# Optimization experiments

Hardware: AMD Instinct MI355X
Metric: run time of the kernel (lower is better)

Reference implementation:

```python
import jax, jax.numpy as jnp
import numpy as np
from jax import lax

B, T, D, NH = 8, 2048, 128, 4
HD = D // NH
EPS = 1e-5


def _ln(x, g, b):
    m = x.mean(-1, keepdims=True)
    v = ((x - m) ** 2).mean(-1, keepdims=True)
    return (x - m) / jnp.sqrt(v + EPS) * g + b


def _gelu(x):  # exact (erf) GELU, matching torch nn.GELU default
    return jax.nn.gelu(x, approximate=False)


def _forward(lob_feat, trade_feat, has_trade,
             ei_w, ei_b, ei_g, ei_beta, decay,
             in_proj_w, in_proj_b, out_proj_w, out_proj_b,
             cn_g, cn_b,
             lob_w, lob_b, lob_g, lob_beta,
             tr_w, tr_b, tr_g, tr_beta,
             of_w, of_b, of_g, of_beta):
    # event impact: Linear -> LayerNorm -> Tanh, gated by has_trade
    impact = jnp.tanh(_ln(trade_feat @ ei_w.T + ei_b, ei_g, ei_beta))
    impact = impact * has_trade[..., None]              # [B,T,D]

    # diagonal linear recurrence: state_t = sigmoid(decay) * state_{t-1} + impact_t
    d = jax.nn.sigmoid(decay)                           # [D]

    def step(s, x):
        s = d * s + x
        return s, s

    _, states = lax.scan(step, jnp.zeros_like(impact[:, 0]),
                         jnp.swapaxes(impact, 0, 1))    # [T,B,D]
    state_seq = jnp.swapaxes(states, 0, 1)              # [B,T,D]

    # fusion MLPs (dropout is identity in eval)
    lob_enh = _gelu(_ln(jnp.concatenate([lob_feat, state_seq], -1) @ lob_w.T + lob_b,
                        lob_g, lob_beta))
    trade_enh = _gelu(_ln(jnp.concatenate([trade_feat, state_seq], -1) @ tr_w.T + tr_b,
                          tr_g, tr_beta))

    # torch nn.MultiheadAttention (batch_first): q=lob_enh, k=v=trade_enh
    wq, wk, wv = in_proj_w[:D], in_proj_w[D:2 * D], in_proj_w[2 * D:]
    bq, bk, bv = in_proj_b[:D], in_proj_b[D:2 * D], in_proj_b[2 * D:]
    q = (lob_enh @ wq.T + bq).reshape(B, T, NH, HD)
    k = (trade_enh @ wk.T + bk).reshape(B, T, NH, HD)
    v = (trade_enh @ wv.T + bv).reshape(B, T, NH, HD)
    scores = jnp.einsum('bqhd,bkhd->bhqk', q, k) / jnp.sqrt(jnp.float32(HD))
    attn = jax.nn.softmax(scores, axis=-1)
    ctx = jnp.einsum('bhqk,bkhd->bqhd', attn, v).reshape(B, T, D)
    fused_attn = ctx @ out_proj_w.T + out_proj_b

    fused = _ln(lob_enh + fused_attn, cn_g, cn_b)
    output = _gelu(_ln(jnp.concatenate([fused, trade_enh], -1) @ of_w.T + of_b,
                       of_g, of_beta))
    return output


def setup_inputs() -> dict:
    key = jax.random.key(0)
    ks = jax.random.split(key, 20)
    s1 = 1.0 / np.sqrt(D)
    s2 = 1.0 / np.sqrt(2 * D)
    return {
        'lob_feat': jax.random.normal(ks[0], (B, T, D), jnp.float32),
        'trade_feat': jax.random.normal(ks[1], (B, T, D), jnp.float32),
        'has_trade': (jax.random.uniform(ks[2], (B, T)) < 0.5).astype(jnp.float32),
        'ei_w': jax.random.normal(ks[3], (D, D), jnp.float32) * s1,
        'ei_b': jnp.zeros((D,), jnp.float32),
        'ei_g': jnp.ones((D,), jnp.float32),
        'ei_beta': jnp.zeros((D,), jnp.float32),
        'decay': jnp.ones((D,), jnp.float32) * 0.9,
        'in_proj_w': jax.random.normal(ks[4], (3 * D, D), jnp.float32) * s1,
        'in_proj_b': jnp.zeros((3 * D,), jnp.float32),
        'out_proj_w': jax.random.normal(ks[5], (D, D), jnp.float32) * s1,
        'out_proj_b': jnp.zeros((D,), jnp.float32),
        'cn_g': jnp.ones((D,), jnp.float32),
        'cn_b': jnp.zeros((D,), jnp.float32),
        'lob_w': jax.random.normal(ks[6], (D, 2 * D), jnp.float32) * s2,
        'lob_b': jnp.zeros((D,), jnp.float32),
        'lob_g': jnp.ones((D,), jnp.float32),
        'lob_beta': jnp.zeros((D,), jnp.float32),
        'tr_w': jax.random.normal(ks[7], (D, 2 * D), jnp.float32) * s2,
        'tr_b': jnp.zeros((D,), jnp.float32),
        'tr_g': jnp.ones((D,), jnp.float32),
        'tr_beta': jnp.zeros((D,), jnp.float32),
        'of_w': jax.random.normal(ks[8], (D, 2 * D), jnp.float32) * s2,
        'of_b': jnp.zeros((D,), jnp.float32),
        'of_g': jnp.ones((D,), jnp.float32),
        'of_beta': jnp.zeros((D,), jnp.float32),
    }


def reference(lob_feat, trade_feat, has_trade,
              ei_w, ei_b, ei_g, ei_beta, decay,
              in_proj_w, in_proj_b, out_proj_w, out_proj_b,
              cn_g, cn_b,
              lob_w, lob_b, lob_g, lob_beta,
              tr_w, tr_b, tr_g, tr_beta,
              of_w, of_b, of_g, of_beta):
    return _forward(lob_feat, trade_feat, has_trade,
                    ei_w, ei_b, ei_g, ei_beta, decay,
                    in_proj_w, in_proj_b, out_proj_w, out_proj_b,
                    cn_g, cn_b,
                    lob_w, lob_b, lob_g, lob_beta,
                    tr_w, tr_b, tr_g, tr_beta,
                    of_w, of_b, of_g, of_beta)
```

## Files before the change

kernel.cpp:

```cpp
#include <hip/hip_runtime.h>
#include <math.h>


#define T_  2048

typedef short bf16x8 __attribute__((ext_vector_type(8)));
typedef float f32x4  __attribute__((ext_vector_type(4)));
typedef unsigned short ushort_t;

__device__ __forceinline__ float sigm(float x) { return 1.0f / (1.0f + __expf(-x)); }

__device__ __forceinline__ unsigned short f2bf(float x) {
    union { float f; unsigned u; } v; v.f = x;
    unsigned r = v.u + 0x7FFFu + ((v.u >> 16) & 1u);
    return (unsigned short)(r >> 16);
}
__device__ __forceinline__ float bf2f(ushort_t u) {
    union { unsigned u; float f; } v; v.u = ((unsigned)u) << 16; return v.f;
}

__device__ __forceinline__ float gelu_f(float x) {
    const float e = exp2f(fmaf(0.044715f * x, x * x, x) * -2.3022083f);
    return x * __builtin_amdgcn_rcpf(1.0f + e);
}
__device__ __forceinline__ float tanh_f(float y) {
    const float e = exp2f(y * 2.8853900818f);
    return 1.0f - 2.0f * __builtin_amdgcn_rcpf(e + 1.0f);
}
#define MX3(a, b, c) fmaxf(fmaxf((a), (b)), (c))

__global__ __launch_bounds__(256) void prep_kernel(
    const float* __restrict__ lob, const float* __restrict__ trade,
    const float* __restrict__ eiw, const float* __restrict__ ipw,
    const float* __restrict__ opw, const float* __restrict__ lobw,
    const float* __restrict__ trw, const float* __restrict__ ofw,
    ushort_t* __restrict__ pool)
{
    const size_t i8 = ((size_t)blockIdx.x * 256 + threadIdx.x) * 8;
    const float* src; size_t off;
    if      (i8 < 2097152) { src = lob;   off = 0; }
    else if (i8 < 4194304) { src = trade; off = 2097152; }
    else if (i8 < 4210688) { src = eiw;   off = 4194304; }
    else if (i8 < 4259840) { src = ipw;   off = 4210688; }
    else if (i8 < 4276224) { src = opw;   off = 4259840; }
    else if (i8 < 4308992) { src = lobw;  off = 4276224; }
    else if (i8 < 4341760) { src = trw;   off = 4308992; }
    else                   { src = ofw;   off = 4341760; }
    const float4 a = *(const float4*)(src + (i8 - off));
    const float4 b = *(const float4*)(src + (i8 - off) + 4);
    bf16x8 o;
    o[0] = (short)f2bf(a.x); o[1] = (short)f2bf(a.y);
    o[2] = (short)f2bf(a.z); o[3] = (short)f2bf(a.w);
    o[4] = (short)f2bf(b.x); o[5] = (short)f2bf(b.y);
    o[6] = (short)f2bf(b.z); o[7] = (short)f2bf(b.w);
    *(bf16x8*)(pool + i8) = o;
}

__global__ __launch_bounds__(256) void gemm_ei(
    const ushort_t* __restrict__ Xb0, const ushort_t* __restrict__ Wb,
    const float* __restrict__ bias, const float* __restrict__ gamma,
    const float* __restrict__ beta, const float* __restrict__ extra,
    ushort_t* __restrict__ outb)
{
    __shared__ float red[32][2][2];
    const int tid = threadIdx.x, wid = tid >> 6, lane = tid & 63;
    const int c2 = lane & 15, g = lane >> 4;
    const int rowblk = wid >> 1, chf = wid & 1, cb0 = chf * 4;
    const int R0 = blockIdx.x * 32 + rowblk * 16;

    f32x4 acc[4] = {};
#pragma unroll
    for (int ch = 0; ch < 4; ch++) {
        const bf16x8 a = *(const bf16x8*)(Xb0 + (size_t)(R0 + c2) * 128 + ch * 32 + g * 8);
#pragma unroll
        for (int j = 0; j < 4; j++) {
            const bf16x8 b = *(const bf16x8*)(Wb + (size_t)((cb0 + j) * 16 + c2) * 128 + ch * 32 + g * 8);
            acc[j] = __builtin_amdgcn_mfma_f32_16x16x32_bf16(a, b, acc[j], 0, 0, 0);
        }
    }
    float gm[4], bt[4];
#pragma unroll
    for (int j = 0; j < 4; j++) {
        const int col = (cb0 + j) * 16 + c2;
        const float bb = bias[col];
        gm[j] = gamma[col]; bt[j] = beta[col];
#pragma unroll
        for (int r = 0; r < 4; r++) acc[j][r] += bb;
    }
#pragma unroll
    for (int r = 0; r < 4; r++) {
        float s = 0.f, ss = 0.f;
#pragma unroll
        for (int j = 0; j < 4; j++) { const float v = acc[j][r]; s += v; ss = fmaf(v, v, ss); }
#pragma unroll
        for (int o = 8; o; o >>= 1) { s += __shfl_xor(s, o); ss += __shfl_xor(ss, o); }
        if (c2 == 0) {
            red[rowblk * 16 + 4 * g + r][chf][0] = s;
            red[rowblk * 16 + 4 * g + r][chf][1] = ss;
        }
    }
    __syncthreads();
#pragma unroll
    for (int r = 0; r < 4; r++) {
        const int lr = rowblk * 16 + 4 * g + r;
        const float S  = red[lr][0][0] + red[lr][1][0];
        const float SS = red[lr][0][1] + red[lr][1][1];
        const float mean = S * (1.0f / 128.0f);
        float var = SS * (1.0f / 128.0f) - mean * mean;
        var = fmaxf(var, 0.0f);
        const float rstd = rsqrtf(var + 1e-5f);
        const int R = blockIdx.x * 32 + lr;
        const float ext = extra[R];
#pragma unroll
        for (int j = 0; j < 4; j++) {
            const float y = (acc[j][r] - mean) * rstd * gm[j] + bt[j];
            outb[(size_t)R * 128 + (cb0 + j) * 16 + c2] = f2bf(tanh_f(y) * ext);
        }
    }
}

__global__ __launch_bounds__(256) void enh_qkv(
    const ushort_t* __restrict__ lobb, const ushort_t* __restrict__ trab,
    const ushort_t* __restrict__ stab,
    const ushort_t* __restrict__ lobw, const ushort_t* __restrict__ trw,
    const ushort_t* __restrict__ ipw, const float* __restrict__ ipb,
    const float* __restrict__ lob_b, const float* __restrict__ lob_g,
    const float* __restrict__ lob_beta,
    const float* __restrict__ tr_b, const float* __restrict__ tr_g,
    const float* __restrict__ tr_beta,
    ushort_t* __restrict__ lobe_b, ushort_t* __restrict__ tre_bf,
    ushort_t* __restrict__ qo, ushort_t* __restrict__ ko, ushort_t* __restrict__ vo)
{
    __shared__ ushort_t lob_t[32][136];
    __shared__ ushort_t tre_t[32][136];
    __shared__ ushort_t vls[128][36];
    __shared__ float red[32][2][4];
    const int tid = threadIdx.x, wid = tid >> 6, lane = tid & 63;
    const int c2 = lane & 15, g = lane >> 4;
    const int rowblk = wid >> 1, chf = wid & 1, cb0 = chf * 4;
    const int RB = blockIdx.x * 32;
    const int R0 = RB + rowblk * 16;

    f32x4 aL[4] = {}, aT[4] = {};
#pragma unroll
    for (int ch = 0; ch < 8; ch++) {
        const int kk = (ch & 3) * 32;
        bf16x8 xl, xt;
        if (ch < 4) {
            xl = *(const bf16x8*)(lobb + (size_t)(R0 + c2) * 128 + kk + g * 8);
            xt = *(const bf16x8*)(trab + (size_t)(R0 + c2) * 128 + kk + g * 8);
        } else {
            xl = *(const bf16x8*)(stab + (size_t)(R0 + c2) * 128 + kk + g * 8);
            xt = xl;
        }
#pragma unroll
        for (int j = 0; j < 4; j++) {
            const size_t wo = (size_t)((cb0 + j) * 16 + c2) * 256 + ch * 32 + g * 8;
            aL[j] = __builtin_amdgcn_mfma_f32_16x16x32_bf16(xl, *(const bf16x8*)(lobw + wo), aL[j], 0, 0, 0);
            aT[j] = __builtin_amdgcn_mfma_f32_16x16x32_bf16(xt, *(const bf16x8*)(trw + wo), aT[j], 0, 0, 0);
        }
    }
#pragma unroll
    for (int j = 0; j < 4; j++) {
        const int col = (cb0 + j) * 16 + c2;
        const float bL = lob_b[col], bT = tr_b[col];
#pragma unroll
        for (int r = 0; r < 4; r++) { aL[j][r] += bL; aT[j][r] += bT; }
    }
#pragma unroll
    for (int r = 0; r < 4; r++) {
        float sL = 0.f, ssL = 0.f, sT = 0.f, ssT = 0.f;
#pragma unroll
        for (int j = 0; j < 4; j++) {
            const float vL = aL[j][r], vT = aT[j][r];
            sL += vL; ssL = fmaf(vL, vL, ssL);
            sT += vT; ssT = fmaf(vT, vT, ssT);
        }
#pragma unroll
        for (int o = 8; o; o >>= 1) {
            sL += __shfl_xor(sL, o); ssL += __shfl_xor(ssL, o);
            sT += __shfl_xor(sT, o); ssT += __shfl_xor(ssT, o);
        }
        if (c2 == 0) {
            float* rd = red[rowblk * 16 + 4 * g + r][chf];
            rd[0] = sL; rd[1] = ssL; rd[2] = sT; rd[3] = ssT;
        }
    }
    __syncthreads();
#pragma unroll
    for (int r = 0; r < 4; r++) {
        const int lr = rowblk * 16 + 4 * g + r;
        const int R = RB + lr;
        const float SL  = red[lr][0][0] + red[lr][1][0];
        const float SSL = red[lr][0][1] + red[lr][1][1];
        const float ST  = red[lr][0][2] + red[lr][1][2];
        const float SST = red[lr][0][3] + red[lr][1][3];
        const float mL = SL * (1.0f / 128.0f), mT = ST * (1.0f / 128.0f);
        const float rL = rsqrtf(fmaxf(SSL * (1.0f / 128.0f) - mL * mL, 0.0f) + 1e-5f);
        const float rT = rsqrtf(fmaxf(SST * (1.0f / 128.0f) - mT * mT, 0.0f) + 1e-5f);
#pragma unroll
        for (int j = 0; j < 4; j++) {
            const int col = (cb0 + j) * 16 + c2;
            const float yL = gelu_f((aL[j][r] - mL) * rL * lob_g[col] + lob_beta[col]);
            const float yT = gelu_f((aT[j][r] - mT) * rT * tr_g[col] + tr_beta[col]);
            const ushort_t lb = f2bf(yL);
            lobe_b[(size_t)R * 128 + col] = lb;
            lob_t[lr][col] = lb;
            const ushort_t tb = f2bf(yT);
            tre_bf[(size_t)R * 128 + col] = tb;
            tre_t[lr][col] = tb;
        }
    }
    __syncthreads();

    const float qscale = 0.17677669529663687f * 1.4426950408889634f;
#pragma unroll
    for (int which = 0; which < 3; which++) {
        const ushort_t (*src)[136] = (which == 0) ? lob_t : tre_t;
        const ushort_t* Wp = ipw + (size_t)which * 16384;
        f32x4 pa[4] = {};
#pragma unroll
        for (int ch = 0; ch < 4; ch++) {
            const bf16x8 a = *(const bf16x8*)&src[rowblk * 16 + c2][ch * 32 + g * 8];
#pragma unroll
            for (int j = 0; j < 4; j++) {
                const bf16x8 b = *(const bf16x8*)(Wp + (size_t)((cb0 + j) * 16 + c2) * 128 + ch * 32 + g * 8);
                pa[j] = __builtin_amdgcn_mfma_f32_16x16x32_bf16(a, b, pa[j], 0, 0, 0);
            }
        }
        if (which < 2) {
            ushort_t* dst = (which == 0) ? qo : ko;
            const float sc = (which == 0) ? qscale : 1.0f;
#pragma unroll
            for (int j = 0; j < 4; j++) {
                const int col = (cb0 + j) * 16 + c2;
                const float bb = ipb[which * 128 + col];
                const int h = col >> 5, hd = col & 31;
#pragma unroll
                for (int r = 0; r < 4; r++) {
                    const int R = R0 + 4 * g + r;
                    const int b = R >> 11, t = R & 2047;
                    dst[(((size_t)b * 4 + h) * 2048 + t) * 32 + hd] = f2bf((pa[j][r] + bb) * sc);
                }
            }
        } else {
#pragma unroll
            for (int j = 0; j < 4; j++) {
                const int col = (cb0 + j) * 16 + c2;
                const float bb = ipb[256 + col];
#pragma unroll
                for (int r = 0; r < 4; r++)
                    vls[col][rowblk * 16 + 4 * g + r] = f2bf(pa[j][r] + bb);
            }
        }
    }
    __syncthreads();
    {
        const int col = tid >> 1, hf = tid & 1;
        const int h = col >> 5, hd = col & 31;
        const int b = RB >> 11;
        unsigned w[8];
#pragma unroll
        for (int e = 0; e < 8; e++) {
            const int p0 = hf * 16 + 2 * e;
            const int g2 = p0 >> 3, j2 = p0 & 7;
            const int lk = 4 * g2 + j2 + (j2 >= 4 ? 12 : 0);
            w[e] = (unsigned)vls[col][lk] | ((unsigned)vls[col][lk + 1] << 16);
        }
        ushort_t* dst = vo + (((size_t)b * 4 + h) * 32 + hd) * 2048 + (RB & 2047) + hf * 16;
        *(uint4*)dst       = *(const uint4*)&w[0];
        *(uint4*)(dst + 8) = *(const uint4*)&w[4];
    }
}

__global__ __launch_bounds__(256) void attn_kernel(
    const ushort_t* __restrict__ q, const ushort_t* __restrict__ k,
    const ushort_t* __restrict__ vtg,
    ushort_t* __restrict__ part, float* __restrict__ rs_part,
    float* __restrict__ m_part)
{
    __shared__ ushort_t ks[2][64][40];
    __shared__ ushort_t vt[2][32][72];
    const int tid = threadIdx.x, wid = tid >> 6, lane = tid & 63;
    const int c = lane & 15, g = lane >> 4;
    const int half = blockIdx.x & 1, qt = blockIdx.x >> 1;
    const int bh = blockIdx.y, b = bh >> 2, h = bh & 3;
    const ushort_t* kb_ = k   + (size_t)bh * 65536 + (size_t)half * 1024 * 32;
    const ushort_t* vb_ = vtg + (size_t)bh * 65536 + (size_t)half * 1024;
    const int q0 = qt * 128 + wid * 32;

    const ushort_t* qbase = q + ((size_t)bh * 2048 + q0) * 32;
    const bf16x8 qf0 = *(const bf16x8*)(qbase + (size_t)c * 32 + g * 8);
    const bf16x8 qf1 = *(const bf16x8*)(qbase + (size_t)(16 + c) * 32 + g * 8);

    bf16x8 ones;
#pragma unroll
    for (int i = 0; i < 8; i++) ones[i] = (short)0x3F80;

    float m0 = 0.0f, m1 = 0.0f;
    f32x4 acc[2][2] = {};
    f32x4 racc[2] = {};

    const int srow = tid >> 2, ssg = tid & 3;
    const int vd = tid >> 3, vkg = tid & 7;

    {
        const bf16x8 kk8 = *(const bf16x8*)(kb_ + (size_t)srow * 32 + ssg * 8);
        const bf16x8 vv8 = *(const bf16x8*)(vb_ + (size_t)vd * 2048 + vkg * 8);
        *(bf16x8*)&ks[0][srow][ssg * 8] = kk8;
        *(bf16x8*)&vt[0][vd][vkg * 8] = vv8;
    }
    __syncthreads();

    for (int kt = 0; kt < 16; kt++) {
        const int cur = kt & 1;
        bf16x8 kk8, vv8;
        if (kt + 1 < 16) {
            kk8 = *(const bf16x8*)(kb_ + ((size_t)(kt + 1) * 64 + srow) * 32 + ssg * 8);
            vv8 = *(const bf16x8*)(vb_ + (size_t)vd * 2048 + (kt + 1) * 64 + vkg * 8);
        }

        f32x4 s0[4], s1[4];
        __builtin_amdgcn_s_setprio(1);
#pragma unroll
        for (int kb2 = 0; kb2 < 4; kb2++) {
            const bf16x8 kf = *(const bf16x8*)&ks[cur][kb2 * 16 + c][g * 8];
            f32x4 z = {};
            s0[kb2] = __builtin_amdgcn_mfma_f32_16x16x32_bf16(kf, qf0, z, 0, 0, 0);
            s1[kb2] = __builtin_amdgcn_mfma_f32_16x16x32_bf16(kf, qf1, z, 0, 0, 0);
        }
        __builtin_amdgcn_s_setprio(0);

        float lm = MX3(s0[0][0], s0[0][1], s0[0][2]);
        lm = MX3(lm, s0[0][3], s0[1][0]);
        lm = MX3(lm, s0[1][1], s0[1][2]);
        lm = MX3(lm, s0[1][3], s0[2][0]);
        lm = MX3(lm, s0[2][1], s0[2][2]);
        lm = MX3(lm, s0[2][3], s0[3][0]);
        lm = MX3(lm, s0[3][1], s0[3][2]);
        lm = MX3(lm, s0[3][3], s1[0][0]);
        lm = MX3(lm, s1[0][1], s1[0][2]);
        lm = MX3(lm, s1[0][3], s1[1][0]);
        lm = MX3(lm, s1[1][1], s1[1][2]);
        lm = MX3(lm, s1[1][3], s1[2][0]);
        lm = MX3(lm, s1[2][1], s1[2][2]);
        lm = MX3(lm, s1[2][3], s1[3][0]);
        lm = MX3(lm, s1[3][1], s1[3][2]);
        lm = fmaxf(lm, s1[3][3]);
        if (__any(lm > 80.0f || m0 != 0.0f || m1 != 0.0f)) {
            float l0 = -1e30f, l1 = -1e30f;
#pragma unroll
            for (int kb2 = 0; kb2 < 4; kb2++) {
#pragma unroll
                for (int r = 0; r < 4; r++) { l0 = fmaxf(l0, s0[kb2][r]); l1 = fmaxf(l1, s1[kb2][r]); }
            }
            l0 = fmaxf(l0, __shfl_xor(l0, 16)); l0 = fmaxf(l0, __shfl_xor(l0, 32));
            l1 = fmaxf(l1, __shfl_xor(l1, 16)); l1 = fmaxf(l1, __shfl_xor(l1, 32));
            const float n0 = fmaxf(m0, l0), n1 = fmaxf(m1, l1);
            const float a0 = exp2f(m0 - n0), a1 = exp2f(m1 - n1);
#pragma unroll
            for (int nb = 0; nb < 2; nb++)
#pragma unroll
                for (int r = 0; r < 4; r++) { acc[0][nb][r] *= a0; acc[1][nb][r] *= a1; }
#pragma unroll
            for (int r = 0; r < 4; r++) { racc[0][r] *= a0; racc[1][r] *= a1; }
            m0 = n0; m1 = n1;
#pragma unroll
            for (int kb2 = 0; kb2 < 4; kb2++)
#pragma unroll
                for (int r = 0; r < 4; r++) {
                    s0[kb2][r] = exp2f(s0[kb2][r] - m0);
                    s1[kb2][r] = exp2f(s1[kb2][r] - m1);
                }
        } else {
#pragma unroll
            for (int kb2 = 0; kb2 < 4; kb2++)
#pragma unroll
                for (int r = 0; r < 4; r++) {
                    s0[kb2][r] = exp2f(s0[kb2][r]);
                    s1[kb2][r] = exp2f(s1[kb2][r]);
                }
        }

        union { unsigned u[4]; bf16x8 v; } p0a, p0b, p1a, p1b;
        asm("v_cvt_pk_bf16_f32 %0, %1, %2" : "=v"(p0a.u[0]) : "v"(s0[0][0]), "v"(s0[0][1]));
        asm("v_cvt_pk_bf16_f32 %0, %1, %2" : "=v"(p0a.u[1]) : "v"(s0[0][2]), "v"(s0[0][3]));
        asm("v_cvt_pk_bf16_f32 %0, %1, %2" : "=v"(p0a.u[2]) : "v"(s0[1][0]), "v"(s0[1][1]));
        asm("v_cvt_pk_bf16_f32 %0, %1, %2" : "=v"(p0a.u[3]) : "v"(s0[1][2]), "v"(s0[1][3]));
        asm("v_cvt_pk_bf16_f32 %0, %1, %2" : "=v"(p0b.u[0]) : "v"(s0[2][0]), "v"(s0[2][1]));
        asm("v_cvt_pk_bf16_f32 %0, %1, %2" : "=v"(p0b.u[1]) : "v"(s0[2][2]), "v"(s0[2][3]));
        asm("v_cvt_pk_bf16_f32 %0, %1, %2" : "=v"(p0b.u[2]) : "v"(s0[3][0]), "v"(s0[3][1]));
        asm("v_cvt_pk_bf16_f32 %0, %1, %2" : "=v"(p0b.u[3]) : "v"(s0[3][2]), "v"(s0[3][3]));
        asm("v_cvt_pk_bf16_f32 %0, %1, %2" : "=v"(p1a.u[0]) : "v"(s1[0][0]), "v"(s1[0][1]));
        asm("v_cvt_pk_bf16_f32 %0, %1, %2" : "=v"(p1a.u[1]) : "v"(s1[0][2]), "v"(s1[0][3]));
        asm("v_cvt_pk_bf16_f32 %0, %1, %2" : "=v"(p1a.u[2]) : "v"(s1[1][0]), "v"(s1[1][1]));
        asm("v_cvt_pk_bf16_f32 %0, %1, %2" : "=v"(p1a.u[3]) : "v"(s1[1][2]), "v"(s1[1][3]));
        asm("v_cvt_pk_bf16_f32 %0, %1, %2" : "=v"(p1b.u[0]) : "v"(s1[2][0]), "v"(s1[2][1]));
        asm("v_cvt_pk_bf16_f32 %0, %1, %2" : "=v"(p1b.u[1]) : "v"(s1[2][2]), "v"(s1[2][3]));
        asm("v_cvt_pk_bf16_f32 %0, %1, %2" : "=v"(p1b.u[2]) : "v"(s1[3][0]), "v"(s1[3][1]));
        asm("v_cvt_pk_bf16_f32 %0, %1, %2" : "=v"(p1b.u[3]) : "v"(s1[3][2]), "v"(s1[3][3]));

        __builtin_amdgcn_s_setprio(1);
#pragma unroll
        for (int nb = 0; nb < 2; nb++) {
            const bf16x8 v0 = *(const bf16x8*)&vt[cur][nb * 16 + c][g * 8];
            const bf16x8 v1 = *(const bf16x8*)&vt[cur][nb * 16 + c][32 + g * 8];
            acc[0][nb] = __builtin_amdgcn_mfma_f32_16x16x32_bf16(v0, p0a.v, acc[0][nb], 0, 0, 0);
            acc[0][nb] = __builtin_amdgcn_mfma_f32_16x16x32_bf16(v1, p0b.v, acc[0][nb], 0, 0, 0);
            acc[1][nb] = __builtin_amdgcn_mfma_f32_16x16x32_bf16(v0, p1a.v, acc[1][nb], 0, 0, 0);
            acc[1][nb] = __builtin_amdgcn_mfma_f32_16x16x32_bf16(v1, p1b.v, acc[1][nb], 0, 0, 0);
        }
        racc[0] = __builtin_amdgcn_mfma_f32_16x16x32_bf16(ones, p0a.v, racc[0], 0, 0, 0);
        racc[0] = __builtin_amdgcn_mfma_f32_16x16x32_bf16(ones, p0b.v, racc[0], 0, 0, 0);
        racc[1] = __builtin_amdgcn_mfma_f32_16x16x32_bf16(ones, p1a.v, racc[1], 0, 0, 0);
        racc[1] = __builtin_amdgcn_mfma_f32_16x16x32_bf16(ones, p1b.v, racc[1], 0, 0, 0);
        __builtin_amdgcn_s_setprio(0);

        if (kt + 1 < 16) {
            *(bf16x8*)&ks[cur ^ 1][srow][ssg * 8] = kk8;
            *(bf16x8*)&vt[cur ^ 1][vd][vkg * 8] = vv8;
        }
        __syncthreads();
    }

    ushort_t* pb = part + (size_t)half * 2097152;
#pragma unroll
    for (int qf = 0; qf < 2; qf++) {
        const int qrow = q0 + qf * 16 + c;
        ushort_t* dst = pb + ((size_t)(b * 2048 + qrow)) * 128 + h * 32;
#pragma unroll
        for (int nb = 0; nb < 2; nb++) {
            unsigned w0, w1;
            asm("v_cvt_pk_bf16_f32 %0, %1, %2" : "=v"(w0) : "v"(acc[qf][nb][0]), "v"(acc[qf][nb][1]));
            asm("v_cvt_pk_bf16_f32 %0, %1, %2" : "=v"(w1) : "v"(acc[qf][nb][2]), "v"(acc[qf][nb][3]));
            uint2 wv; wv.x = w0; wv.y = w1;
            *(uint2*)(dst + nb * 16 + 4 * g) = wv;
        }
    }
    if (g == 0) {
        float* rsp = rs_part + (size_t)(half * 32 + bh) * 2048;
        float* mp  = m_part  + (size_t)(half * 32 + bh) * 2048;
        rsp[q0 + c]      = racc[0][0];
        rsp[q0 + 16 + c] = racc[1][0];
        mp[q0 + c]       = m0;
        mp[q0 + 16 + c]  = m1;
    }
}

__global__ __launch_bounds__(256) void out_fuse(
    const ushort_t* __restrict__ ctxA, const ushort_t* __restrict__ ctxB,
    const float* __restrict__ rs_part, const float* __restrict__ m_part,
    const ushort_t* __restrict__ treb,
    const ushort_t* __restrict__ opw, const float* __restrict__ opb,
    const float* __restrict__ cn_g, const float* __restrict__ cn_b,
    const ushort_t* __restrict__ ofw, const float* __restrict__ of_b,
    const float* __restrict__ of_g, const float* __restrict__ of_beta,
    const ushort_t* __restrict__ lobe_b, float* __restrict__ out)
{
    __shared__ ushort_t fus_t[32][136];
    __shared__ float red[32][2][2];
    const int tid = threadIdx.x, wid = tid >> 6, lane = tid & 63;
    const int c2 = lane & 15, g = lane >> 4;
    const int rowblk = wid >> 1, chf = wid & 1, cb0 = chf * 4;
    const int RB = blockIdx.x * 32;
    const int R0 = RB + rowblk * 16;

    const int rowA = R0 + c2;
    const int bb2 = rowA >> 11, tt = rowA & 2047;
    float fA[4], fB[4];
#pragma unroll
    for (int h = 0; h < 4; h++) {
        const int bh = bb2 * 4 + h;
        const float mA = m_part[(size_t)bh * 2048 + tt];
        const float mB = m_part[(size_t)(32 + bh) * 2048 + tt];
        const float rA = rs_part[(size_t)bh * 2048 + tt];
        const float rB = rs_part[(size_t)(32 + bh) * 2048 + tt];
        const float M = fmaxf(mA, mB);
        const float wA = exp2f(mA - M), wB = exp2f(mB - M);
        const float inv = __builtin_amdgcn_rcpf(fmaf(rA, wA, rB * wB));
        fA[h] = wA * inv; fB[h] = wB * inv;
    }

    f32x4 acc[4] = {};
#pragma unroll
    for (int ch = 0; ch < 4; ch++) {
        const bf16x8 aA = *(const bf16x8*)(ctxA + (size_t)rowA * 128 + ch * 32 + g * 8);
        const bf16x8 aB = *(const bf16x8*)(ctxB + (size_t)rowA * 128 + ch * 32 + g * 8);
        union { unsigned u[4]; bf16x8 v; } am;
#pragma unroll
        for (int i = 0; i < 4; i++) {
            const float e0 = bf2f((ushort_t)aA[2 * i]) * fA[ch] + bf2f((ushort_t)aB[2 * i]) * fB[ch];
            const float e1 = bf2f((ushort_t)aA[2 * i + 1]) * fA[ch] + bf2f((ushort_t)aB[2 * i + 1]) * fB[ch];
            asm("v_cvt_pk_bf16_f32 %0, %1, %2" : "=v"(am.u[i]) : "v"(e0), "v"(e1));
        }
#pragma unroll
        for (int j = 0; j < 4; j++) {
            const bf16x8 b = *(const bf16x8*)(opw + (size_t)((cb0 + j) * 16 + c2) * 128 + ch * 32 + g * 8);
            acc[j] = __builtin_amdgcn_mfma_f32_16x16x32_bf16(am.v, b, acc[j], 0, 0, 0);
        }
    }
#pragma unroll
    for (int j = 0; j < 4; j++) {
        const int col = (cb0 + j) * 16 + c2;
        const float bb = opb[col];
#pragma unroll
        for (int r = 0; r < 4; r++)
            acc[j][r] += bb + bf2f(lobe_b[(size_t)(R0 + 4 * g + r) * 128 + col]);
    }
#pragma unroll
    for (int r = 0; r < 4; r++) {
        float s = 0.f, ss = 0.f;
#pragma unroll
        for (int j = 0; j < 4; j++) { const float v = acc[j][r]; s += v; ss = fmaf(v, v, ss); }
#pragma unroll
        for (int o = 8; o; o >>= 1) { s += __shfl_xor(s, o); ss += __shfl_xor(ss, o); }
        if (c2 == 0) {
            red[rowblk * 16 + 4 * g + r][chf][0] = s;
            red[rowblk * 16 + 4 * g + r][chf][1] = ss;
        }
    }
    __syncthreads();
#pragma unroll
    for (int r = 0; r < 4; r++) {
        const int lr = rowblk * 16 + 4 * g + r;
        const float S  = red[lr][0][0] + red[lr][1][0];
        const float SS = red[lr][0][1] + red[lr][1][1];
        const float mean = S * (1.0f / 128.0f);
        const float rstd = rsqrtf(fmaxf(SS * (1.0f / 128.0f) - mean * mean, 0.0f) + 1e-5f);
#pragma unroll
        for (int j = 0; j < 4; j++) {
            const int col = (cb0 + j) * 16 + c2;
            fus_t[lr][col] = f2bf((acc[j][r] - mean) * rstd * cn_g[col] + cn_b[col]);
        }
    }
    __syncthreads();

    f32x4 a2[4] = {};
#pragma unroll
    for (int ch = 0; ch < 8; ch++) {
        bf16x8 a;
        if (ch < 4) a = *(const bf16x8*)&fus_t[rowblk * 16 + c2][ch * 32 + g * 8];
        else        a = *(const bf16x8*)(treb + (size_t)(R0 + c2) * 128 + (ch - 4) * 32 + g * 8);
#pragma unroll
        for (int j = 0; j < 4; j++) {
            const bf16x8 b = *(const bf16x8*)(ofw + (size_t)((cb0 + j) * 16 + c2) * 256 + ch * 32 + g * 8);
            a2[j] = __builtin_amdgcn_mfma_f32_16x16x32_bf16(a, b, a2[j], 0, 0, 0);
        }
    }
#pragma unroll
    for (int j = 0; j < 4; j++) {
        const float bb = of_b[(cb0 + j) * 16 + c2];
#pragma unroll
        for (int r = 0; r < 4; r++) a2[j][r] += bb;
    }
#pragma unroll
    for (int r = 0; r < 4; r++) {
        float s = 0.f, ss = 0.f;
#pragma unroll
        for (int j = 0; j < 4; j++) { const float v = a2[j][r]; s += v; ss = fmaf(v, v, ss); }
#pragma unroll
        for (int o = 8; o; o >>= 1) { s += __shfl_xor(s, o); ss += __shfl_xor(ss, o); }
        if (c2 == 0) {
            red[rowblk * 16 + 4 * g + r][chf][0] = s;
            red[rowblk * 16 + 4 * g + r][chf][1] = ss;
        }
    }
    __syncthreads();
#pragma unroll
    for (int r = 0; r < 4; r++) {
        const int lr = rowblk * 16 + 4 * g + r;
        const float S  = red[lr][0][0] + red[lr][1][0];
        const float SS = red[lr][0][1] + red[lr][1][1];
        const float mean = S * (1.0f / 128.0f);
        const float rstd = rsqrtf(fmaxf(SS * (1.0f / 128.0f) - mean * mean, 0.0f) + 1e-5f);
        const int R = RB + lr;
#pragma unroll
        for (int j = 0; j < 4; j++) {
            const int col = (cb0 + j) * 16 + c2;
            const float y = (a2[j][r] - mean) * rstd * of_g[col] + of_beta[col];
            out[(size_t)R * 128 + col] = gelu_f(y);
        }
    }
}

__global__ void scan_ends_kernel(const ushort_t* __restrict__ imp,
                                 const float* __restrict__ decay,
                                 float* __restrict__ ends)
{
    const int c = threadIdx.x;
    const int ch = blockIdx.x, b = blockIdx.y;
    const float d = sigm(decay[c]);
    const size_t base = ((size_t)b * T_ + ch * 64) * 128 + c;
    float s = 0.0f;
#pragma unroll 4
    for (int tl = 0; tl < 64; tl++)
        s = fmaf(d, s, bf2f(imp[base + (size_t)tl * 128]));
    ends[((size_t)b * 32 + ch) * 128 + c] = s;
}

__global__ void scan_carry_kernel(const float* __restrict__ ends,
                                  const float* __restrict__ decay,
                                  float* __restrict__ carry)
{
    const int c = threadIdx.x;
    const int b = blockIdx.x;
    const float d = sigm(decay[c]);
    float dl = d;
#pragma unroll
    for (int i = 0; i < 6; i++) dl *= dl;
    float e = 0.0f;
#pragma unroll
    for (int ch = 0; ch < 32; ch++) {
        carry[((size_t)b * 32 + ch) * 128 + c] = e;
        e = fmaf(dl, e, ends[((size_t)b * 32 + ch) * 128 + c]);
    }
}

__global__ void scan_fin_kernel(const ushort_t* __restrict__ imp,
                                const float* __restrict__ decay,
                                const float* __restrict__ carry,
                                ushort_t* __restrict__ stbf)
{
    const int c = threadIdx.x;
    const int ch = blockIdx.x, b = blockIdx.y;
    const float d = sigm(decay[c]);
    float s = carry[((size_t)b * 32 + ch) * 128 + c];
    const size_t base = ((size_t)b * T_ + ch * 64) * 128 + c;
#pragma unroll 4
    for (int tl = 0; tl < 64; tl++) {
        s = fmaf(d, s, bf2f(imp[base + (size_t)tl * 128]));
        stbf[base + (size_t)tl * 128] = f2bf(s);
    }
}

extern "C" void kernel_launch(void* const* d_in, const int* in_sizes, int n_in,
                              void* d_out, int out_size, void* d_ws, size_t ws_size,
                              hipStream_t stream)
{
    const float* lob_feat   = (const float*)d_in[0];
    const float* trade_feat = (const float*)d_in[1];
    const float* has_trade  = (const float*)d_in[2];
    const float* ei_w       = (const float*)d_in[3];
    const float* ei_b       = (const float*)d_in[4];
    const float* ei_g       = (const float*)d_in[5];
    const float* ei_beta    = (const float*)d_in[6];
    const float* decay      = (const float*)d_in[7];
    const float* in_proj_w  = (const float*)d_in[8];
    const float* in_proj_b  = (const float*)d_in[9];
    const float* out_proj_w = (const float*)d_in[10];
    const float* out_proj_b = (const float*)d_in[11];
    const float* cn_g       = (const float*)d_in[12];
    const float* cn_b       = (const float*)d_in[13];
    const float* lob_w      = (const float*)d_in[14];
    const float* lob_b      = (const float*)d_in[15];
    const float* lob_g      = (const float*)d_in[16];
    const float* lob_beta   = (const float*)d_in[17];
    const float* tr_w       = (const float*)d_in[18];
    const float* tr_b       = (const float*)d_in[19];
    const float* tr_g       = (const float*)d_in[20];
    const float* tr_beta    = (const float*)d_in[21];
    const float* of_w       = (const float*)d_in[22];
    const float* of_b       = (const float*)d_in[23];
    const float* of_g       = (const float*)d_in[24];
    const float* of_beta    = (const float*)d_in[25];

    char* W = (char*)d_ws;
    const size_t MB = 1u << 20;
    ushort_t* lobe_b   = (ushort_t*)W;
    float*    carry    = (float*)(W + 8 * MB);
    float*    ends     = (float*)(W + 8 * MB + 256 * 1024);
    ushort_t* pool     = (ushort_t*)(W + 9 * MB);
    ushort_t* imp_bf   = (ushort_t*)(W + 18 * MB);
    ushort_t* state_bf = (ushort_t*)(W + 22 * MB);
    ushort_t* tre_bf   = (ushort_t*)(W + 26 * MB);
    ushort_t* q_bf     = (ushort_t*)(W + 30 * MB);
    ushort_t* k_bf     = (ushort_t*)(W + 34 * MB);
    ushort_t* vt_g     = (ushort_t*)(W + 38 * MB);
    ushort_t* part     = (ushort_t*)(W + 42 * MB);
    float*    rs_part  = (float*)(W + 50 * MB);
    float*    m_part   = (float*)(W + 50 * MB + 512 * 1024);

    ushort_t* lob_bf   = pool;
    ushort_t* trade_bf = pool + 2097152;
    ushort_t* eiw_bf   = pool + 4194304;
    ushort_t* ipw_bf   = pool + 4210688;
    ushort_t* opw_bf   = pool + 4259840;
    ushort_t* lobw_bf  = pool + 4276224;
    ushort_t* trw_bf   = pool + 4308992;
    ushort_t* ofw_bf   = pool + 4341760;

    ushort_t* ctxA = part;
    ushort_t* ctxB = part + 2097152;

    const dim3 blk(256);

    prep_kernel<<<dim3(2136), blk, 0, stream>>>(lob_feat, trade_feat, ei_w, in_proj_w,
                                                out_proj_w, lob_w, tr_w, of_w, pool);
    gemm_ei<<<dim3(512), blk, 0, stream>>>(trade_bf, eiw_bf, ei_b, ei_g, ei_beta,
                                           has_trade, imp_bf);
    scan_ends_kernel<<<dim3(32, 8), dim3(128), 0, stream>>>(imp_bf, decay, ends);
    scan_carry_kernel<<<dim3(8), dim3(128), 0, stream>>>(ends, decay, carry);
    scan_fin_kernel<<<dim3(32, 8), dim3(128), 0, stream>>>(imp_bf, decay, carry, state_bf);
    enh_qkv<<<dim3(512), blk, 0, stream>>>(lob_bf, trade_bf, state_bf, lobw_bf, trw_bf,
                                           ipw_bf, in_proj_b, lob_b, lob_g, lob_beta,
                                           tr_b, tr_g, tr_beta, lobe_b, tre_bf,
                                           q_bf, k_bf, vt_g);
    attn_kernel<<<dim3(32, 32), blk, 0, stream>>>(q_bf, k_bf, vt_g, part, rs_part, m_part);
    out_fuse<<<dim3(512), blk, 0, stream>>>(ctxA, ctxB, rs_part, m_part, tre_bf,
                                            opw_bf, out_proj_b, cn_g, cn_b,
                                            ofw_bf, of_b, of_g, of_beta, lobe_b, (float*)d_out);
}
```

Before: 139.7 us.

## Split attention keys into four chunks and process query halves sequentially

The attention kernel now splits the key dimension four ways instead of two, doubling the grid to 2048 blocks, each handling 512 keys. out_fuse merges four partial contexts with a log-sum-exp style reweighting. The inner loop also processes the two 16-row query fragments one after another rather than interleaved, which lowers live register pressure. The goal is higher occupancy and more parallelism on the attention stage. The cost is more partial-result traffic and a heavier merge, and the workspace is relaid out with imp_bf aliased onto the part buffer.

```diff
diff --git a/kernel.cpp b/kernel.cpp
--- a/kernel.cpp
+++ b/kernel.cpp
@@ -283,10 +283,10 @@
     __shared__ ushort_t vt[2][32][72];
     const int tid = threadIdx.x, wid = tid >> 6, lane = tid & 63;
     const int c = lane & 15, g = lane >> 4;
-    const int half = blockIdx.x & 1, qt = blockIdx.x >> 1;
+    const int kq = blockIdx.x & 3, qt = blockIdx.x >> 2;
     const int bh = blockIdx.y, b = bh >> 2, h = bh & 3;
-    const ushort_t* kb_ = k   + (size_t)bh * 65536 + (size_t)half * 1024 * 32;
-    const ushort_t* vb_ = vtg + (size_t)bh * 65536 + (size_t)half * 1024;
+    const ushort_t* kb_ = k   + (size_t)bh * 65536 + (size_t)kq * 512 * 32;
+    const ushort_t* vb_ = vtg + (size_t)bh * 65536 + (size_t)kq * 512;
     const int q0 = qt * 128 + wid * 32;
 
     const ushort_t* qbase = q + ((size_t)bh * 2048 + q0) * 32;
@@ -312,118 +312,144 @@
     }
     __syncthreads();
 
-    for (int kt = 0; kt < 16; kt++) {
+    for (int kt = 0; kt < 8; kt++) {
         const int cur = kt & 1;
         bf16x8 kk8, vv8;
-        if (kt + 1 < 16) {
+        if (kt + 1 < 8) {
             kk8 = *(const bf16x8*)(kb_ + ((size_t)(kt + 1) * 64 + srow) * 32 + ssg * 8);
             vv8 = *(const bf16x8*)(vb_ + (size_t)vd * 2048 + (kt + 1) * 64 + vkg * 8);
         }
 
-        f32x4 s0[4], s1[4];
-        __builtin_amdgcn_s_setprio(1);
-#pragma unroll
-        for (int kb2 = 0; kb2 < 4; kb2++) {
-            const bf16x8 kf = *(const bf16x8*)&ks[cur][kb2 * 16 + c][g * 8];
-            f32x4 z = {};
-            s0[kb2] = __builtin_amdgcn_mfma_f32_16x16x32_bf16(kf, qf0, z, 0, 0, 0);
-            s1[kb2] = __builtin_amdgcn_mfma_f32_16x16x32_bf16(kf, qf1, z, 0, 0, 0);
-        }
-        __builtin_amdgcn_s_setprio(0);
-
-        float lm = MX3(s0[0][0], s0[0][1], s0[0][2]);
-        lm = MX3(lm, s0[0][3], s0[1][0]);
-        lm = MX3(lm, s0[1][1], s0[1][2]);
-        lm = MX3(lm, s0[1][3], s0[2][0]);
-        lm = MX3(lm, s0[2][1], s0[2][2]);
-        lm = MX3(lm, s0[2][3], s0[3][0]);
-        lm = MX3(lm, s0[3][1], s0[3][2]);
-        lm = MX3(lm, s0[3][3], s1[0][0]);
-        lm = MX3(lm, s1[0][1], s1[0][2]);
-        lm = MX3(lm, s1[0][3], s1[1][0]);
-        lm = MX3(lm, s1[1][1], s1[1][2]);
-        lm = MX3(lm, s1[1][3], s1[2][0]);
-        lm = MX3(lm, s1[2][1], s1[2][2]);
-        lm = MX3(lm, s1[2][3], s1[3][0]);
-        lm = MX3(lm, s1[3][1], s1[3][2]);
-        lm = fmaxf(lm, s1[3][3]);
-        if (__any(lm > 80.0f || m0 != 0.0f || m1 != 0.0f)) {
-            float l0 = -1e30f, l1 = -1e30f;
+        {
+            f32x4 s[4];
+            __builtin_amdgcn_s_setprio(1);
 #pragma unroll
             for (int kb2 = 0; kb2 < 4; kb2++) {
-#pragma unroll
-                for (int r = 0; r < 4; r++) { l0 = fmaxf(l0, s0[kb2][r]); l1 = fmaxf(l1, s1[kb2][r]); }
-            }
-            l0 = fmaxf(l0, __shfl_xor(l0, 16)); l0 = fmaxf(l0, __shfl_xor(l0, 32));
-            l1 = fmaxf(l1, __shfl_xor(l1, 16)); l1 = fmaxf(l1, __shfl_xor(l1, 32));
-            const float n0 = fmaxf(m0, l0), n1 = fmaxf(m1, l1);
-            const float a0 = exp2f(m0 - n0), a1 = exp2f(m1 - n1);
-#pragma unroll
-            for (int nb = 0; nb < 2; nb++)
-#pragma unroll
-                for (int r = 0; r < 4; r++) { acc[0][nb][r] *= a0; acc[1][nb][r] *= a1; }
-#pragma unroll
-            for (int r = 0; r < 4; r++) { racc[0][r] *= a0; racc[1][r] *= a1; }
-            m0 = n0; m1 = n1;
-#pragma unroll
-            for (int kb2 = 0; kb2 < 4; kb2++)
-#pragma unroll
-                for (int r = 0; r < 4; r++) {
-                    s0[kb2][r] = exp2f(s0[kb2][r] - m0);
-                    s1[kb2][r] = exp2f(s1[kb2][r] - m1);
-                }
-        } else {
-#pragma unroll
-            for (int kb2 = 0; kb2 < 4; kb2++)
-#pragma unroll
-                for (int r = 0; r < 4; r++) {
-                    s0[kb2][r] = exp2f(s0[kb2][r]);
-                    s1[kb2][r] = exp2f(s1[kb2][r]);
-                }
-        }
-
-        union { unsigned u[4]; bf16x8 v; } p0a, p0b, p1a, p1b;
-        asm("v_cvt_pk_bf16_f32 %0, %1, %2" : "=v"(p0a.u[0]) : "v"(s0[0][0]), "v"(s0[0][1]));
-        asm("v_cvt_pk_bf16_f32 %0, %1, %2" : "=v"(p0a.u[1]) : "v"(s0[0][2]), "v"(s0[0][3]));
-        asm("v_cvt_pk_bf16_f32 %0, %1, %2" : "=v"(p0a.u[2]) : "v"(s0[1][0]), "v"(s0[1][1]));
-        asm("v_cvt_pk_bf16_f32 %0, %1, %2" : "=v"(p0a.u[3]) : "v"(s0[1][2]), "v"(s0[1][3]));
-        asm("v_cvt_pk_bf16_f32 %0, %1, %2" : "=v"(p0b.u[0]) : "v"(s0[2][0]), "v"(s0[2][1]));
-        asm("v_cvt_pk_bf16_f32 %0, %1, %2" : "=v"(p0b.u[1]) : "v"(s0[2][2]), "v"(s0[2][3]));
-        asm("v_cvt_pk_bf16_f32 %0, %1, %2" : "=v"(p0b.u[2]) : "v"(s0[3][0]), "v"(s0[3][1]));
-        asm("v_cvt_pk_bf16_f32 %0, %1, %2" : "=v"(p0b.u[3]) : "v"(s0[3][2]), "v"(s0[3][3]));
-        asm("v_cvt_pk_bf16_f32 %0, %1, %2" : "=v"(p1a.u[0]) : "v"(s1[0][0]), "v"(s1[0][1]));
-        asm("v_cvt_pk_bf16_f32 %0, %1, %2" : "=v"(p1a.u[1]) : "v"(s1[0][2]), "v"(s1[0][3]));
-        asm("v_cvt_pk_bf16_f32 %0, %1, %2" : "=v"(p1a.u[2]) : "v"(s1[1][0]), "v"(s1[1][1]));
-        asm("v_cvt_pk_bf16_f32 %0, %1, %2" : "=v"(p1a.u[3]) : "v"(s1[1][2]), "v"(s1[1][3]));
-        asm("v_cvt_pk_bf16_f32 %0, %1, %2" : "=v"(p1b.u[0]) : "v"(s1[2][0]), "v"(s1[2][1]));
-        asm("v_cvt_pk_bf16_f32 %0, %1, %2" : "=v"(p1b.u[1]) : "v"(s1[2][2]), "v"(s1[2][3]));
-        asm("v_cvt_pk_bf16_f32 %0, %1, %2" : "=v"(p1b.u[2]) : "v"(s1[3][0]), "v"(s1[3][1]));
-        asm("v_cvt_pk_bf16_f32 %0, %1, %2" : "=v"(p1b.u[3]) : "v"(s1[3][2]), "v"(s1[3][3]));
-
-        __builtin_amdgcn_s_setprio(1);
-#pragma unroll
-        for (int nb = 0; nb < 2; nb++) {
-            const bf16x8 v0 = *(const bf16x8*)&vt[cur][nb * 16 + c][g * 8];
-            const bf16x8 v1 = *(const bf16x8*)&vt[cur][nb * 16 + c][32 + g * 8];
-            acc[0][nb] = __builtin_amdgcn_mfma_f32_16x16x32_bf16(v0, p0a.v, acc[0][nb], 0, 0, 0);
-            acc[0][nb] = __builtin_amdgcn_mfma_f32_16x16x32_bf16(v1, p0b.v, acc[0][nb], 0, 0, 0);
-            acc[1][nb] = __builtin_amdgcn_mfma_f32_16x16x32_bf16(v0, p1a.v, acc[1][nb], 0, 0, 0);
-            acc[1][nb] = __builtin_amdgcn_mfma_f32_16x16x32_bf16(v1, p1b.v, acc[1][nb], 0, 0, 0);
-        }
-        racc[0] = __builtin_amdgcn_mfma_f32_16x16x32_bf16(ones, p0a.v, racc[0], 0, 0, 0);
-        racc[0] = __builtin_amdgcn_mfma_f32_16x16x32_bf16(ones, p0b.v, racc[0], 0, 0, 0);
-        racc[1] = __builtin_amdgcn_mfma_f32_16x16x32_bf16(ones, p1a.v, racc[1], 0, 0, 0);
-        racc[1] = __builtin_amdgcn_mfma_f32_16x16x32_bf16(ones, p1b.v, racc[1], 0, 0, 0);
-        __builtin_amdgcn_s_setprio(0);
-
-        if (kt + 1 < 16) {
+                const bf16x8 kf = *(const bf16x8*)&ks[cur][kb2 * 16 + c][g * 8];
+                f32x4 z = {};
+                s[kb2] = __builtin_amdgcn_mfma_f32_16x16x32_bf16(kf, qf0, z, 0, 0, 0);
+            }
+            __builtin_amdgcn_s_setprio(0);
+            const float t0 = MX3(s[0][0], s[0][1], s[0][2]);
+            const float t1 = MX3(s[0][3], s[1][0], s[1][1]);
+            const float t2 = MX3(s[1][2], s[1][3], s[2][0]);
+            const float t3 = MX3(s[2][1], s[2][2], s[2][3]);
+            const float t4 = MX3(s[3][0], s[3][1], s[3][2]);
+            const float lm = fmaxf(MX3(t0, t1, t2), MX3(t3, t4, s[3][3]));
+            if (__any(lm > 80.0f || m0 != 0.0f)) {
+                float l = lm;
+                l = fmaxf(l, __shfl_xor(l, 16));
+                l = fmaxf(l, __shfl_xor(l, 32));
+                const float n = fmaxf(m0, l);
+                const float a = exp2f(m0 - n);
+#pragma unroll
+                for (int nb = 0; nb < 2; nb++)
+#pragma unroll
+                    for (int r = 0; r < 4; r++) acc[0][nb][r] *= a;
+#pragma unroll
+                for (int r = 0; r < 4; r++) racc[0][r] *= a;
+                m0 = n;
+#pragma unroll
+                for (int kb2 = 0; kb2 < 4; kb2++)
+#pragma unroll
+                    for (int r = 0; r < 4; r++) s[kb2][r] = exp2f(s[kb2][r] - m0);
+            } else {
+#pragma unroll
+                for (int kb2 = 0; kb2 < 4; kb2++)
+#pragma unroll
+                    for (int r = 0; r < 4; r++) s[kb2][r] = exp2f(s[kb2][r]);
+            }
+            union { unsigned u[4]; bf16x8 v; } pa, pb;
+            asm("v_cvt_pk_bf16_f32 %0, %1, %2" : "=v"(pa.u[0]) : "v"(s[0][0]), "v"(s[0][1]));
+            asm("v_cvt_pk_bf16_f32 %0, %1, %2" : "=v"(pa.u[1]) : "v"(s[0][2]), "v"(s[0][3]));
+            asm("v_cvt_pk_bf16_f32 %0, %1, %2" : "=v"(pa.u[2]) : "v"(s[1][0]), "v"(s[1][1]));
+            asm("v_cvt_pk_bf16_f32 %0, %1, %2" : "=v"(pa.u[3]) : "v"(s[1][2]), "v"(s[1][3]));
+            asm("v_cvt_pk_bf16_f32 %0, %1, %2" : "=v"(pb.u[0]) : "v"(s[2][0]), "v"(s[2][1]));
+            asm("v_cvt_pk_bf16_f32 %0, %1, %2" : "=v"(pb.u[1]) : "v"(s[2][2]), "v"(s[2][3]));
+            asm("v_cvt_pk_bf16_f32 %0, %1, %2" : "=v"(pb.u[2]) : "v"(s[3][0]), "v"(s[3][1]));
+            asm("v_cvt_pk_bf16_f32 %0, %1, %2" : "=v"(pb.u[3]) : "v"(s[3][2]), "v"(s[3][3]));
+            __builtin_amdgcn_s_setprio(1);
+#pragma unroll
+            for (int nb = 0; nb < 2; nb++) {
+                const bf16x8 v0 = *(const bf16x8*)&vt[cur][nb * 16 + c][g * 8];
+                const bf16x8 v1 = *(const bf16x8*)&vt[cur][nb * 16 + c][32 + g * 8];
+                acc[0][nb] = __builtin_amdgcn_mfma_f32_16x16x32_bf16(v0, pa.v, acc[0][nb], 0, 0, 0);
+                acc[0][nb] = __builtin_amdgcn_mfma_f32_16x16x32_bf16(v1, pb.v, acc[0][nb], 0, 0, 0);
+            }
+            racc[0] = __builtin_amdgcn_mfma_f32_16x16x32_bf16(ones, pa.v, racc[0], 0, 0, 0);
+            racc[0] = __builtin_amdgcn_mfma_f32_16x16x32_bf16(ones, pb.v, racc[0], 0, 0, 0);
+            __builtin_amdgcn_s_setprio(0);
+        }
+
+        {
+            f32x4 s[4];
+            __builtin_amdgcn_s_setprio(1);
+#pragma unroll
+            for (int kb2 = 0; kb2 < 4; kb2++) {
+                const bf16x8 kf = *(const bf16x8*)&ks[cur][kb2 * 16 + c][g * 8];
+                f32x4 z = {};
+                s[kb2] = __builtin_amdgcn_mfma_f32_16x16x32_bf16(kf, qf1, z, 0, 0, 0);
+            }
+            __builtin_amdgcn_s_setprio(0);
+            const float t0 = MX3(s[0][0], s[0][1], s[0][2]);
+            const float t1 = MX3(s[0][3], s[1][0], s[1][1]);
+            const float t2 = MX3(s[1][2], s[1][3], s[2][0]);
+            const float t3 = MX3(s[2][1], s[2][2], s[2][3]);
+            const float t4 = MX3(s[3][0], s[3][1], s[3][2]);
+            const float lm = fmaxf(MX3(t0, t1, t2), MX3(t3, t4, s[3][3]));
+            if (__any(lm > 80.0f || m1 != 0.0f)) {
+                float l = lm;
+                l = fmaxf(l, __shfl_xor(l, 16));
+                l = fmaxf(l, __shfl_xor(l, 32));
+                const float n = fmaxf(m1, l);
+                const float a = exp2f(m1 - n);
+#pragma unroll
+                for (int nb = 0; nb < 2; nb++)
+#pragma unroll
+                    for (int r = 0; r < 4; r++) acc[1][nb][r] *= a;
+#pragma unroll
+                for (int r = 0; r < 4; r++) racc[1][r] *= a;
+                m1 = n;
+#pragma unroll
+                for (int kb2 = 0; kb2 < 4; kb2++)
+#pragma unroll
+                    for (int r = 0; r < 4; r++) s[kb2][r] = exp2f(s[kb2][r] - m1);
+            } else {
+#pragma unroll
+                for (int kb2 = 0; kb2 < 4; kb2++)
+#pragma unroll
+                    for (int r = 0; r < 4; r++) s[kb2][r] = exp2f(s[kb2][r]);
+            }
+            union { unsigned u[4]; bf16x8 v; } pa, pb;
+            asm("v_cvt_pk_bf16_f32 %0, %1, %2" : "=v"(pa.u[0]) : "v"(s[0][0]), "v"(s[0][1]));
+            asm("v_cvt_pk_bf16_f32 %0, %1, %2" : "=v"(pa.u[1]) : "v"(s[0][2]), "v"(s[0][3]));
+            asm("v_cvt_pk_bf16_f32 %0, %1, %2" : "=v"(pa.u[2]) : "v"(s[1][0]), "v"(s[1][1]));
+            asm("v_cvt_pk_bf16_f32 %0, %1, %2" : "=v"(pa.u[3]) : "v"(s[1][2]), "v"(s[1][3]));
+            asm("v_cvt_pk_bf16_f32 %0, %1, %2" : "=v"(pb.u[0]) : "v"(s[2][0]), "v"(s[2][1]));
+            asm("v_cvt_pk_bf16_f32 %0, %1, %2" : "=v"(pb.u[1]) : "v"(s[2][2]), "v"(s[2][3]));
+            asm("v_cvt_pk_bf16_f32 %0, %1, %2" : "=v"(pb.u[2]) : "v"(s[3][0]), "v"(s[3][1]));
+            asm("v_cvt_pk_bf16_f32 %0, %1, %2" : "=v"(pb.u[3]) : "v"(s[3][2]), "v"(s[3][3]));
+            __builtin_amdgcn_s_setprio(1);
+#pragma unroll
+            for (int nb = 0; nb < 2; nb++) {
+                const bf16x8 v0 = *(const bf16x8*)&vt[cur][nb * 16 + c][g * 8];
+                const bf16x8 v1 = *(const bf16x8*)&vt[cur][nb * 16 + c][32 + g * 8];
+                acc[1][nb] = __builtin_amdgcn_mfma_f32_16x16x32_bf16(v0, pa.v, acc[1][nb], 0, 0, 0);
+                acc[1][nb] = __builtin_amdgcn_mfma_f32_16x16x32_bf16(v1, pb.v, acc[1][nb], 0, 0, 0);
+            }
+            racc[1] = __builtin_amdgcn_mfma_f32_16x16x32_bf16(ones, pa.v, racc[1], 0, 0, 0);
+            racc[1] = __builtin_amdgcn_mfma_f32_16x16x32_bf16(ones, pb.v, racc[1], 0, 0, 0);
+            __builtin_amdgcn_s_setprio(0);
+        }
+
+        if (kt + 1 < 8) {
             *(bf16x8*)&ks[cur ^ 1][srow][ssg * 8] = kk8;
             *(bf16x8*)&vt[cur ^ 1][vd][vkg * 8] = vv8;
         }
         __syncthreads();
     }
 
-    ushort_t* pb = part + (size_t)half * 2097152;
+    ushort_t* pb = part + (size_t)kq * 2097152;
 #pragma unroll
     for (int qf = 0; qf < 2; qf++) {
         const int qrow = q0 + qf * 16 + c;
@@ -438,8 +464,8 @@
         }
     }
     if (g == 0) {
-        float* rsp = rs_part + (size_t)(half * 32 + bh) * 2048;
-        float* mp  = m_part  + (size_t)(half * 32 + bh) * 2048;
+        float* rsp = rs_part + (size_t)(kq * 32 + bh) * 2048;
+        float* mp  = m_part  + (size_t)(kq * 32 + bh) * 2048;
         rsp[q0 + c]      = racc[0][0];
         rsp[q0 + 16 + c] = racc[1][0];
         mp[q0 + c]       = m0;
@@ -448,7 +474,7 @@
 }
 
 __global__ __launch_bounds__(256) void out_fuse(
-    const ushort_t* __restrict__ ctxA, const ushort_t* __restrict__ ctxB,
+    const ushort_t* __restrict__ part,
     const float* __restrict__ rs_part, const float* __restrict__ m_part,
     const ushort_t* __restrict__ treb,
     const ushort_t* __restrict__ opw, const float* __restrict__ opb,
@@ -467,30 +493,41 @@
 
     const int rowA = R0 + c2;
     const int bb2 = rowA >> 11, tt = rowA & 2047;
-    float fA[4], fB[4];
+    float f[4][4];
 #pragma unroll
     for (int h = 0; h < 4; h++) {
         const int bh = bb2 * 4 + h;
-        const float mA = m_part[(size_t)bh * 2048 + tt];
-        const float mB = m_part[(size_t)(32 + bh) * 2048 + tt];
-        const float rA = rs_part[(size_t)bh * 2048 + tt];
-        const float rB = rs_part[(size_t)(32 + bh) * 2048 + tt];
-        const float M = fmaxf(mA, mB);
-        const float wA = exp2f(mA - M), wB = exp2f(mB - M);
-        const float inv = __builtin_amdgcn_rcpf(fmaf(rA, wA, rB * wB));
-        fA[h] = wA * inv; fB[h] = wB * inv;
+        float m[4], r[4];
+#pragma unroll
+        for (int s = 0; s < 4; s++) {
+            m[s] = m_part[(size_t)(s * 32 + bh) * 2048 + tt];
+            r[s] = rs_part[(size_t)(s * 32 + bh) * 2048 + tt];
+        }
+        const float M = fmaxf(fmaxf(m[0], m[1]), fmaxf(m[2], m[3]));
+        float w[4], den = 0.f;
+#pragma unroll
+        for (int s = 0; s < 4; s++) { w[s] = exp2f(m[s] - M); den = fmaf(r[s], w[s], den); }
+        const float inv = __builtin_amdgcn_rcpf(den);
+#pragma unroll
+        for (int s = 0; s < 4; s++) f[s][h] = w[s] * inv;
     }
 
     f32x4 acc[4] = {};
 #pragma unroll
     for (int ch = 0; ch < 4; ch++) {
-        const bf16x8 aA = *(const bf16x8*)(ctxA + (size_t)rowA * 128 + ch * 32 + g * 8);
-        const bf16x8 aB = *(const bf16x8*)(ctxB + (size_t)rowA * 128 + ch * 32 + g * 8);
+        bf16x8 a[4];
+#pragma unroll
+        for (int s = 0; s < 4; s++)
+            a[s] = *(const bf16x8*)(part + (size_t)s * 2097152 + (size_t)rowA * 128 + ch * 32 + g * 8);
         union { unsigned u[4]; bf16x8 v; } am;
 #pragma unroll
         for (int i = 0; i < 4; i++) {
-            const float e0 = bf2f((ushort_t)aA[2 * i]) * fA[ch] + bf2f((ushort_t)aB[2 * i]) * fB[ch];
-            const float e1 = bf2f((ushort_t)aA[2 * i + 1]) * fA[ch] + bf2f((ushort_t)aB[2 * i + 1]) * fB[ch];
+            float e0 = 0.f, e1 = 0.f;
+#pragma unroll
+            for (int s = 0; s < 4; s++) {
+                e0 = fmaf(bf2f((ushort_t)a[s][2 * i]), f[s][ch], e0);
+                e1 = fmaf(bf2f((ushort_t)a[s][2 * i + 1]), f[s][ch], e1);
+            }
             asm("v_cvt_pk_bf16_f32 %0, %1, %2" : "=v"(am.u[i]) : "v"(e0), "v"(e1));
         }
 #pragma unroll
@@ -667,18 +704,18 @@
     char* W = (char*)d_ws;
     const size_t MB = 1u << 20;
     ushort_t* lobe_b   = (ushort_t*)W;
-    float*    carry    = (float*)(W + 8 * MB);
-    float*    ends     = (float*)(W + 8 * MB + 256 * 1024);
-    ushort_t* pool     = (ushort_t*)(W + 9 * MB);
-    ushort_t* imp_bf   = (ushort_t*)(W + 18 * MB);
-    ushort_t* state_bf = (ushort_t*)(W + 22 * MB);
-    ushort_t* tre_bf   = (ushort_t*)(W + 26 * MB);
-    ushort_t* q_bf     = (ushort_t*)(W + 30 * MB);
-    ushort_t* k_bf     = (ushort_t*)(W + 34 * MB);
-    ushort_t* vt_g     = (ushort_t*)(W + 38 * MB);
-    ushort_t* part     = (ushort_t*)(W + 42 * MB);
+    ushort_t* state_bf = (ushort_t*)(W + 4 * MB);
+    ushort_t* tre_bf   = (ushort_t*)(W + 8 * MB);
+    ushort_t* q_bf     = (ushort_t*)(W + 12 * MB);
+    ushort_t* k_bf     = (ushort_t*)(W + 16 * MB);
+    ushort_t* vt_g     = (ushort_t*)(W + 20 * MB);
+    ushort_t* pool     = (ushort_t*)(W + 24 * MB);
+    float*    carry    = (float*)(W + 33 * MB);
+    float*    ends     = (float*)(W + 33 * MB + 256 * 1024);
+    ushort_t* part     = (ushort_t*)(W + 34 * MB);
+    ushort_t* imp_bf   = part;
     float*    rs_part  = (float*)(W + 50 * MB);
-    float*    m_part   = (float*)(W + 50 * MB + 512 * 1024);
+    float*    m_part   = (float*)(W + 51 * MB);
 
     ushort_t* lob_bf   = pool;
     ushort_t* trade_bf = pool + 2097152;
@@ -688,9 +725,6 @@
     ushort_t* lobw_bf  = pool + 4276224;
     ushort_t* trw_bf   = pool + 4308992;
     ushort_t* ofw_bf   = pool + 4341760;
-
-    ushort_t* ctxA = part;
-    ushort_t* ctxB = part + 2097152;
 
     const dim3 blk(256);
 
@@ -705,8 +739,8 @@
                                            ipw_bf, in_proj_b, lob_b, lob_g, lob_beta,
                                            tr_b, tr_g, tr_beta, lobe_b, tre_bf,
                                            q_bf, k_bf, vt_g);
-    attn_kernel<<<dim3(32, 32), blk, 0, stream>>>(q_bf, k_bf, vt_g, part, rs_part, m_part);
-    out_fuse<<<dim3(512), blk, 0, stream>>>(ctxA, ctxB, rs_part, m_part, tre_bf,
+    attn_kernel<<<dim3(64, 32), blk, 0, stream>>>(q_bf, k_bf, vt_g, part, rs_part, m_part);
+    out_fuse<<<dim3(512), blk, 0, stream>>>(part, rs_part, m_part, tre_bf,
                                             opw_bf, out_proj_b, cn_g, cn_b,
                                             ofw_bf, of_b, of_g, of_beta, lobe_b, (float*)d_out);
 }
```

Result: no change. 141.6 us (+1.4%).
